# Kernel tuning notes

Hardware: AMD Instinct MI355X
Metric: run time of the kernel (lower is better)

Reference implementation:

```python
import jax, jax.numpy as jnp
import numpy as np

N_STATE = 1024
N_HEAD = 16
DIM_PER_HEAD = N_STATE // N_HEAD  # 64
QK_SCALE = DIM_PER_HEAD ** (-0.5)
B, T, T_CACHE = 8, 256, 768


def setup_inputs() -> dict:
    key = jax.random.key(0)
    ks = jax.random.split(key, 12)
    s = 0.02
    return {
        "x": jax.random.normal(ks[0], (B, T, N_STATE), dtype=jnp.float32),
        "qk_mask": jnp.zeros((T, T_CACHE + T), dtype=jnp.float32),
        "cache_k": jax.random.normal(ks[1], (B, T_CACHE, N_STATE), dtype=jnp.float32),
        "cache_v": jax.random.normal(ks[2], (B, T_CACHE, N_STATE), dtype=jnp.float32),
        "Wq": jax.random.normal(ks[3], (N_STATE, N_STATE), dtype=jnp.float32) * s,
        "bq": jax.random.normal(ks[4], (N_STATE,), dtype=jnp.float32) * s,
        "Wk": jax.random.normal(ks[5], (N_STATE, N_STATE), dtype=jnp.float32) * s,
        "Wv": jax.random.normal(ks[6], (N_STATE, N_STATE), dtype=jnp.float32) * s,
        "bv": jax.random.normal(ks[7], (N_STATE,), dtype=jnp.float32) * s,
        "Wo": jax.random.normal(ks[8], (N_STATE, N_STATE), dtype=jnp.float32) * s,
        "bo": jax.random.normal(ks[9], (N_STATE,), dtype=jnp.float32) * s,
    }


def reference(x, qk_mask, cache_k, cache_v, Wq, bq, Wk, Wv, bv, Wo, bo):
    # Linear projections (weights stored as [in, out], i.e. torch weight^T)
    q = (x @ Wq + bq) * QK_SCALE            # [B, T, D]
    new_k = x @ Wk                           # key has no bias
    new_v = x @ Wv + bv
    # KV-cache concat along time
    k = jnp.concatenate([cache_k, new_k], axis=1)  # [B, Tkv, D]
    v = jnp.concatenate([cache_v, new_v], axis=1)
    # Split heads
    Bq, Tq = q.shape[:2]
    Tkv = k.shape[1]
    qh = q.reshape(Bq, Tq, N_HEAD, DIM_PER_HEAD)    # [B, T, H, d]
    kh = k.reshape(Bq, Tkv, N_HEAD, DIM_PER_HEAD)
    vh = v.reshape(Bq, Tkv, N_HEAD, DIM_PER_HEAD)
    # q @ k^T + mask, softmax over keys
    qk = jnp.einsum("bthd,bshd->bhts", qh, kh) + qk_mask  # [B, H, T, Tkv]
    w = jax.nn.softmax(qk, axis=-1).astype(qh.dtype)
    wv = jnp.einsum("bhts,bshd->bthd", w, vh).reshape(Bq, Tq, N_STATE)
    out = wv @ Wo + bo
    return out, new_k, new_v
```

## Files before the change

kernel.cpp:

```cpp
#include <hip/hip_runtime.h>
#include <hip/hip_bf16.h>
#include <stdint.h>

#define Bb 8
#define Tt 256
#define TCC 768
#define TKV 1024
#define NS 1024
#define NH 16
#define DH 64
#define QK_SCALE 0.125f

typedef short bf16x8 __attribute__((ext_vector_type(8)));
typedef float f32x4 __attribute__((ext_vector_type(4)));

__device__ __forceinline__ unsigned short f2bf(float f) {
  union { float f; uint32_t u; } v; v.f = f;
  uint32_t u = v.u;
  u += 0x7fff + ((u >> 16) & 1);
  return (unsigned short)(u >> 16);
}

__global__ void convert_flat(const float* __restrict__ x, const float* __restrict__ ck,
                             unsigned short* __restrict__ xb, unsigned short* __restrict__ kb) {
  const int64_t nx4 = (int64_t)Bb * Tt * NS / 4;
  const int64_t nk4 = (int64_t)Bb * TCC * NS / 4;
  int64_t stride = (int64_t)gridDim.x * blockDim.x;
  for (int64_t t = (int64_t)blockIdx.x * blockDim.x + threadIdx.x; t < nx4 + nk4; t += stride) {
    if (t < nx4) {
      float4 v = ((const float4*)x)[t];
      ushort4 o; o.x = f2bf(v.x); o.y = f2bf(v.y); o.z = f2bf(v.z); o.w = f2bf(v.w);
      ((ushort4*)xb)[t] = o;
    } else {
      int64_t e = t - nx4;
      float4 v = ((const float4*)ck)[e];
      ushort4 o; o.x = f2bf(v.x); o.y = f2bf(v.y); o.z = f2bf(v.z); o.w = f2bf(v.w);
      int64_t el = e * 4;
      int64_t b = el / ((int64_t)TCC * NS);
      int64_t rem = el % ((int64_t)TCC * NS);
      int64_t d = b * (int64_t)TKV * NS + rem;
      ((ushort4*)kb)[d / 4] = o;
    }
  }
}

__global__ void transpose_convert(const float* __restrict__ Wq, const float* __restrict__ Wk,
                                  const float* __restrict__ Wv, const float* __restrict__ Wo,
                                  const float* __restrict__ cv,
                                  unsigned short* __restrict__ wqt, unsigned short* __restrict__ wkt,
                                  unsigned short* __restrict__ wvt, unsigned short* __restrict__ wot,
                                  unsigned short* __restrict__ vbt) {
  __shared__ float tile[64][65];
  int bid = blockIdx.x;
  const float* src; unsigned short* dst;
  if (bid < 1024) {
    int mat = bid >> 8, t = bid & 255;
    int tr = t >> 4, tc = t & 15;
    const float* W = (mat == 0) ? Wq : (mat == 1) ? Wk : (mat == 2) ? Wv : Wo;
    unsigned short* Wt = (mat == 0) ? wqt : (mat == 1) ? wkt : (mat == 2) ? wvt : wot;
    src = W + (int64_t)(tr * 64) * 1024 + tc * 64;
    dst = Wt + (int64_t)(tc * 64) * 1024 + tr * 64;
  } else {
    int e = bid - 1024;
    int b = e / 192; int t = e % 192;
    int st = t >> 4, ct = t & 15;
    src = cv + (int64_t)b * TCC * NS + (int64_t)(st * 64) * 1024 + ct * 64;
    dst = vbt + (int64_t)b * NS * TKV + (int64_t)(ct * 64) * 1024 + st * 64;
  }
  for (int e = threadIdx.x; e < 4096; e += 256) {
    int i = e >> 6, j = e & 63;
    tile[i][j] = src[(int64_t)i * 1024 + j];
  }
  __syncthreads();
  for (int e = threadIdx.x; e < 4096; e += 256) {
    int i = e >> 6, j = e & 63;
    dst[(int64_t)i * 1024 + j] = f2bf(tile[j][i]);
  }
}

template <int MODE>
__global__ void gemm128(const unsigned short* __restrict__ A,
                        const unsigned short* __restrict__ Bt0, const unsigned short* __restrict__ Bt1,
                        const unsigned short* __restrict__ Bt2,
                        const float* __restrict__ bq, const float* __restrict__ bv,
                        const float* __restrict__ bo,
                        unsigned short* __restrict__ qb,
                        float* __restrict__ okf, float* __restrict__ ovf,
                        unsigned short* __restrict__ kb, unsigned short* __restrict__ vbt,
                        float* __restrict__ outf) {
  __shared__ unsigned short As[128 * 40];
  __shared__ unsigned short Bs[128 * 40];
  int tid = threadIdx.x, lane = tid & 63, w = tid >> 6;
  int lr = lane & 15, hi = lane >> 4;
  int wr = w >> 1, wc = w & 1;

  int tm, seg, col0;
  const unsigned short* Bt;
  if (MODE == 0) {
    tm = blockIdx.x & 15; int tn = blockIdx.x >> 4;
    seg = tn >> 3; col0 = (tn & 7) * 128;
    Bt = (seg == 0) ? Bt0 : (seg == 1) ? Bt1 : Bt2;
  } else {
    tm = blockIdx.x & 15; int tn = blockIdx.x >> 4;
    seg = 0; col0 = tn * 128;
    Bt = Bt0;
  }
  int m0 = tm * 128;

  f32x4 acc[4][4];
#pragma unroll
  for (int i = 0; i < 4; i++)
#pragma unroll
    for (int j = 0; j < 4; j++) acc[i][j] = (f32x4){0.f, 0.f, 0.f, 0.f};

  for (int k0 = 0; k0 < 1024; k0 += 32) {
#pragma unroll
    for (int e = tid; e < 512; e += 256) {
      int r = e >> 2, kc = (e & 3) * 8;
      *(bf16x8*)&As[r * 40 + kc] = *(const bf16x8*)&A[(int64_t)(m0 + r) * 1024 + k0 + kc];
      *(bf16x8*)&Bs[r * 40 + kc] = *(const bf16x8*)&Bt[(int64_t)(col0 + r) * 1024 + k0 + kc];
    }
    __syncthreads();
    bf16x8 af[4], bf[4];
#pragma unroll
    for (int mt = 0; mt < 4; mt++) af[mt] = *(const bf16x8*)&As[(wr * 64 + mt * 16 + lr) * 40 + hi * 8];
#pragma unroll
    for (int nt = 0; nt < 4; nt++) bf[nt] = *(const bf16x8*)&Bs[(wc * 64 + nt * 16 + lr) * 40 + hi * 8];
#pragma unroll
    for (int mt = 0; mt < 4; mt++)
#pragma unroll
      for (int nt = 0; nt < 4; nt++)
        acc[mt][nt] = __builtin_amdgcn_mfma_f32_16x16x32_bf16(af[mt], bf[nt], acc[mt][nt], 0, 0, 0);
    __syncthreads();
  }

#pragma unroll
  for (int mt = 0; mt < 4; mt++)
#pragma unroll
    for (int nt = 0; nt < 4; nt++) {
      int row = m0 + wr * 64 + mt * 16 + hi * 4;
      int col = col0 + wc * 64 + nt * 16 + lr;
      if (MODE == 1) {
        float bias = bo[col];
#pragma unroll
        for (int r = 0; r < 4; r++)
          outf[(int64_t)(row + r) * 1024 + col] = acc[mt][nt][r] + bias;
      } else if (seg == 0) {
        float bias = bq[col];
#pragma unroll
        for (int r = 0; r < 4; r++)
          qb[(int64_t)(row + r) * 1024 + col] = f2bf((acc[mt][nt][r] + bias) * QK_SCALE);
      } else if (seg == 1) {
#pragma unroll
        for (int r = 0; r < 4; r++) {
          float v = acc[mt][nt][r];
          okf[(int64_t)(row + r) * 1024 + col] = v;
          int b = (row + r) >> 8, t = (row + r) & 255;
          kb[((int64_t)(b * TKV + TCC + t)) * 1024 + col] = f2bf(v);
        }
      } else {
        float bias = bv[col];
        int b = row >> 8, t0 = row & 255;
        int64_t voff = ((int64_t)(b * NH + (col >> 6)) * DH + (col & 63)) * TKV + TCC + t0;
        ushort4 pk;
        float v0 = acc[mt][nt][0] + bias, v1 = acc[mt][nt][1] + bias,
              v2 = acc[mt][nt][2] + bias, v3 = acc[mt][nt][3] + bias;
        ovf[(int64_t)(row + 0) * 1024 + col] = v0;
        ovf[(int64_t)(row + 1) * 1024 + col] = v1;
        ovf[(int64_t)(row + 2) * 1024 + col] = v2;
        ovf[(int64_t)(row + 3) * 1024 + col] = v3;
        pk.x = f2bf(v0); pk.y = f2bf(v1); pk.z = f2bf(v2); pk.w = f2bf(v3);
        *(ushort4*)&vbt[voff] = pk;
      }
    }
}

__global__ void attn(const unsigned short* __restrict__ qb, const unsigned short* __restrict__ kb,
                     const unsigned short* __restrict__ vbt, const float* __restrict__ mask,
                     unsigned short* __restrict__ wvb) {
  __shared__ unsigned short Ks[64 * 72];
  __shared__ unsigned short Vs[64 * 72];
  __shared__ unsigned short Ps[4][16 * 72];
  int tid = threadIdx.x, lane = tid & 63, w = tid >> 6;
  int lr = lane & 15, hi = lane >> 4;
  int qblk = blockIdx.x & 3, bh = blockIdx.x >> 2, b = bh >> 4, h = bh & 15;
  int q0 = qblk * 64 + w * 16;

  const unsigned short* qp = qb + ((int64_t)(b * Tt + q0 + lr)) * 1024 + h * DH + hi * 8;
  bf16x8 aq0 = *(const bf16x8*)qp;
  bf16x8 aq1 = *(const bf16x8*)(qp + 32);

  f32x4 o[4];
#pragma unroll
  for (int nt = 0; nt < 4; nt++) o[nt] = (f32x4){0.f, 0.f, 0.f, 0.f};
  float m[4] = {-1e30f, -1e30f, -1e30f, -1e30f};
  float l[4] = {0.f, 0.f, 0.f, 0.f};

  const unsigned short* kbase = kb + (int64_t)b * TKV * 1024 + h * DH;
  const unsigned short* vbase = vbt + (int64_t)bh * DH * TKV;
  const float* mbase = mask + (int64_t)(q0 + hi * 4) * TKV;

  for (int c = 0; c < 16; c++) {
    int kv0 = c * 64;
#pragma unroll
    for (int e = tid; e < 512; e += 256) {
      int r = e >> 3, kc = (e & 7) * 8;
      *(bf16x8*)&Ks[r * 72 + kc] = *(const bf16x8*)&kbase[(int64_t)(kv0 + r) * 1024 + kc];
      *(bf16x8*)&Vs[r * 72 + kc] = *(const bf16x8*)&vbase[(int64_t)r * TKV + kv0 + kc];
    }
    __syncthreads();

    f32x4 s[4];
#pragma unroll
    for (int nt = 0; nt < 4; nt++) {
      bf16x8 bk0 = *(const bf16x8*)&Ks[(nt * 16 + lr) * 72 + hi * 8];
      bf16x8 bk1 = *(const bf16x8*)&Ks[(nt * 16 + lr) * 72 + 32 + hi * 8];
      f32x4 z = (f32x4){0.f, 0.f, 0.f, 0.f};
      z = __builtin_amdgcn_mfma_f32_16x16x32_bf16(aq0, bk0, z, 0, 0, 0);
      z = __builtin_amdgcn_mfma_f32_16x16x32_bf16(aq1, bk1, z, 0, 0, 0);
      s[nt] = z;
    }
#pragma unroll
    for (int nt = 0; nt < 4; nt++)
#pragma unroll
      for (int r = 0; r < 4; r++)
        s[nt][r] += mbase[(int64_t)r * TKV + kv0 + nt * 16 + lr];

    float cm[4];
#pragma unroll
    for (int r = 0; r < 4; r++) {
      cm[r] = fmaxf(fmaxf(s[0][r], s[1][r]), fmaxf(s[2][r], s[3][r]));
#pragma unroll
      for (int d = 1; d < 16; d <<= 1) cm[r] = fmaxf(cm[r], __shfl_xor(cm[r], d));
    }
    float al[4], rs[4];
#pragma unroll
    for (int r = 0; r < 4; r++) {
      float nm = fmaxf(m[r], cm[r]);
      al[r] = __expf(m[r] - nm);
      m[r] = nm;
      rs[r] = 0.f;
    }
#pragma unroll
    for (int nt = 0; nt < 4; nt++)
#pragma unroll
      for (int r = 0; r < 4; r++) {
        s[nt][r] = __expf(s[nt][r] - m[r]);
        rs[r] += s[nt][r];
      }
#pragma unroll
    for (int r = 0; r < 4; r++) {
#pragma unroll
      for (int d = 1; d < 16; d <<= 1) rs[r] += __shfl_xor(rs[r], d);
      l[r] = l[r] * al[r] + rs[r];
    }
#pragma unroll
    for (int nt = 0; nt < 4; nt++)
#pragma unroll
      for (int r = 0; r < 4; r++) o[nt][r] *= al[r];

#pragma unroll
    for (int nt = 0; nt < 4; nt++)
#pragma unroll
      for (int r = 0; r < 4; r++)
        Ps[w][(hi * 4 + r) * 72 + nt * 16 + lr] = f2bf(s[nt][r]);
    __syncthreads();

    bf16x8 pa0 = *(const bf16x8*)&Ps[w][lr * 72 + hi * 8];
    bf16x8 pa1 = *(const bf16x8*)&Ps[w][lr * 72 + 32 + hi * 8];
#pragma unroll
    for (int nt = 0; nt < 4; nt++) {
      bf16x8 bv0 = *(const bf16x8*)&Vs[(nt * 16 + lr) * 72 + hi * 8];
      bf16x8 bv1 = *(const bf16x8*)&Vs[(nt * 16 + lr) * 72 + 32 + hi * 8];
      o[nt] = __builtin_amdgcn_mfma_f32_16x16x32_bf16(pa0, bv0, o[nt], 0, 0, 0);
      o[nt] = __builtin_amdgcn_mfma_f32_16x16x32_bf16(pa1, bv1, o[nt], 0, 0, 0);
    }
    __syncthreads();
  }

  float inv[4];
#pragma unroll
  for (int r = 0; r < 4; r++) inv[r] = 1.f / l[r];
#pragma unroll
  for (int nt = 0; nt < 4; nt++)
#pragma unroll
    for (int r = 0; r < 4; r++)
      wvb[(int64_t)(b * Tt + q0 + hi * 4 + r) * 1024 + h * DH + nt * 16 + lr] =
          f2bf(o[nt][r] * inv[r]);
}

extern "C" void kernel_launch(void* const* d_in, const int* in_sizes, int n_in,
                              void* d_out, int out_size, void* d_ws, size_t ws_size,
                              hipStream_t stream) {
  const float* x    = (const float*)d_in[0];
  const float* mask = (const float*)d_in[1];
  const float* ck   = (const float*)d_in[2];
  const float* cv   = (const float*)d_in[3];
  const float* Wq   = (const float*)d_in[4];
  const float* bq   = (const float*)d_in[5];
  const float* Wk   = (const float*)d_in[6];
  const float* Wv   = (const float*)d_in[7];
  const float* bv   = (const float*)d_in[8];
  const float* Wo   = (const float*)d_in[9];
  const float* bo   = (const float*)d_in[10];

  const int64_t NT = (int64_t)Bb * Tt * NS;
  float* outp = (float*)d_out;
  float* okf  = outp + NT;
  float* ovf  = outp + 2 * NT;

  char* ws = (char*)d_ws;
  unsigned short* xb  = (unsigned short*)(ws);
  unsigned short* wqt = (unsigned short*)(ws + (4LL << 20));
  unsigned short* wkt = (unsigned short*)(ws + (6LL << 20));
  unsigned short* wvt = (unsigned short*)(ws + (8LL << 20));
  unsigned short* wot = (unsigned short*)(ws + (10LL << 20));
  unsigned short* qbw = (unsigned short*)(ws + (12LL << 20));
  unsigned short* kbw = (unsigned short*)(ws + (16LL << 20));
  unsigned short* vbt = (unsigned short*)(ws + (32LL << 20));
  unsigned short* wvb = (unsigned short*)(ws + (48LL << 20));

  convert_flat<<<2048, 256, 0, stream>>>(x, ck, xb, kbw);
  transpose_convert<<<2560, 256, 0, stream>>>(Wq, Wk, Wv, Wo, cv, wqt, wkt, wvt, wot, vbt);
  gemm128<0><<<384, 256, 0, stream>>>(xb, wqt, wkt, wvt, bq, bv, bo,
                                      qbw, okf, ovf, kbw, vbt, outp);
  attn<<<512, 256, 0, stream>>>(qbw, kbw, vbt, mask, wvb);
  gemm128<1><<<128, 256, 0, stream>>>(wvb, wot, wot, wot, bq, bv, bo,
                                      qbw, okf, ovf, kbw, vbt, outp);
}
```

Before: 242.7 us.

## Split attention over KV across waves, use direct-to-LDS GEMM loads, vectorize transposes

Attention now gives each block 16 queries and has each of its four waves take a quarter of the KV range, loading K and V fragments straight from global memory. The partial max, sum and output of each wave are merged through shared memory at the end, which removes the per-chunk LDS staging and barriers. The GEMMs use global_load_lds to write tiles directly into unpadded LDS, and the output projection uses 64-row tiles to launch more blocks. The transpose kernel moves to float4 reads and ushort4 writes, and s_setprio is added around the MFMA sections. Unpadded LDS can cause bank conflicts, and per-wave global loads give up reuse of K and V across the waves of a block.

Result: slower. 248.9 us (+2.6%).

```diff
diff --git a/kernel.cpp b/kernel.cpp
--- a/kernel.cpp
+++ b/kernel.cpp
@@ -13,6 +13,7 @@
 
 typedef short bf16x8 __attribute__((ext_vector_type(8)));
 typedef float f32x4 __attribute__((ext_vector_type(4)));
+typedef unsigned int u32;
 
 __device__ __forceinline__ unsigned short f2bf(float f) {
   union { float f; uint32_t u; } v; v.f = f;
@@ -21,8 +22,16 @@
   return (unsigned short)(u >> 16);
 }
 
-__global__ void convert_flat(const float* __restrict__ x, const float* __restrict__ ck,
-                             unsigned short* __restrict__ xb, unsigned short* __restrict__ kb) {
+__device__ __forceinline__ void gload16(const unsigned short* g, unsigned short* l) {
+  __builtin_amdgcn_global_load_lds(
+      (__attribute__((address_space(1))) u32*)g,
+      (__attribute__((address_space(3))) u32*)l,
+      16, 0, 0);
+}
+
+__global__ __launch_bounds__(256) void convert_flat(
+    const float* __restrict__ x, const float* __restrict__ ck,
+    unsigned short* __restrict__ xb, unsigned short* __restrict__ kb) {
   const int64_t nx4 = (int64_t)Bb * Tt * NS / 4;
   const int64_t nk4 = (int64_t)Bb * TCC * NS / 4;
   int64_t stride = (int64_t)gridDim.x * blockDim.x;
@@ -44,12 +53,13 @@
   }
 }
 
-__global__ void transpose_convert(const float* __restrict__ Wq, const float* __restrict__ Wk,
-                                  const float* __restrict__ Wv, const float* __restrict__ Wo,
-                                  const float* __restrict__ cv,
-                                  unsigned short* __restrict__ wqt, unsigned short* __restrict__ wkt,
-                                  unsigned short* __restrict__ wvt, unsigned short* __restrict__ wot,
-                                  unsigned short* __restrict__ vbt) {
+__global__ __launch_bounds__(256) void transpose_convert(
+    const float* __restrict__ Wq, const float* __restrict__ Wk,
+    const float* __restrict__ Wv, const float* __restrict__ Wo,
+    const float* __restrict__ cv,
+    unsigned short* __restrict__ wqt, unsigned short* __restrict__ wkt,
+    unsigned short* __restrict__ wvt, unsigned short* __restrict__ wot,
+    unsigned short* __restrict__ vbt) {
   __shared__ float tile[64][65];
   int bid = blockIdx.x;
   const float* src; unsigned short* dst;
@@ -67,79 +77,95 @@
     src = cv + (int64_t)b * TCC * NS + (int64_t)(st * 64) * 1024 + ct * 64;
     dst = vbt + (int64_t)b * NS * TKV + (int64_t)(ct * 64) * 1024 + st * 64;
   }
-  for (int e = threadIdx.x; e < 4096; e += 256) {
-    int i = e >> 6, j = e & 63;
-    tile[i][j] = src[(int64_t)i * 1024 + j];
+  for (int e = threadIdx.x; e < 1024; e += 256) {
+    int i = e >> 4, j4 = (e & 15) * 4;
+    float4 v = *(const float4*)&src[(int64_t)i * 1024 + j4];
+    tile[i][j4] = v.x; tile[i][j4 + 1] = v.y; tile[i][j4 + 2] = v.z; tile[i][j4 + 3] = v.w;
   }
   __syncthreads();
-  for (int e = threadIdx.x; e < 4096; e += 256) {
-    int i = e >> 6, j = e & 63;
-    dst[(int64_t)i * 1024 + j] = f2bf(tile[j][i]);
+  for (int e = threadIdx.x; e < 1024; e += 256) {
+    int i = e >> 4, j4 = (e & 15) * 4;
+    ushort4 o;
+    o.x = f2bf(tile[j4][i]); o.y = f2bf(tile[j4 + 1][i]);
+    o.z = f2bf(tile[j4 + 2][i]); o.w = f2bf(tile[j4 + 3][i]);
+    *(ushort4*)&dst[(int64_t)i * 1024 + j4] = o;
   }
 }
 
 template <int MODE>
-__global__ void gemm128(const unsigned short* __restrict__ A,
-                        const unsigned short* __restrict__ Bt0, const unsigned short* __restrict__ Bt1,
-                        const unsigned short* __restrict__ Bt2,
-                        const float* __restrict__ bq, const float* __restrict__ bv,
-                        const float* __restrict__ bo,
-                        unsigned short* __restrict__ qb,
-                        float* __restrict__ okf, float* __restrict__ ovf,
-                        unsigned short* __restrict__ kb, unsigned short* __restrict__ vbt,
-                        float* __restrict__ outf) {
-  __shared__ unsigned short As[128 * 40];
-  __shared__ unsigned short Bs[128 * 40];
+__global__ __launch_bounds__(256) void gemm_mfma(
+    const unsigned short* __restrict__ A,
+    const unsigned short* __restrict__ Bt0, const unsigned short* __restrict__ Bt1,
+    const unsigned short* __restrict__ Bt2,
+    const float* __restrict__ bq, const float* __restrict__ bv,
+    const float* __restrict__ bo,
+    unsigned short* __restrict__ qb,
+    float* __restrict__ okf, float* __restrict__ ovf,
+    unsigned short* __restrict__ kb, unsigned short* __restrict__ vbt,
+    float* __restrict__ outf) {
+  constexpr int BM = (MODE == 0) ? 128 : 64;
+  constexpr int NT = (MODE == 0) ? 4 : 2;
+  __shared__ __align__(16) unsigned short As[BM * 32];
+  __shared__ __align__(16) unsigned short Bs[128 * 32];
   int tid = threadIdx.x, lane = tid & 63, w = tid >> 6;
   int lr = lane & 15, hi = lane >> 4;
-  int wr = w >> 1, wc = w & 1;
-
-  int tm, seg, col0;
+  int wr = (MODE == 0) ? (w >> 1) : 0;
+  int colw = (MODE == 0) ? ((w & 1) * 64) : (w * 32);
+
+  int tm, tn, seg, col0;
   const unsigned short* Bt;
   if (MODE == 0) {
-    tm = blockIdx.x & 15; int tn = blockIdx.x >> 4;
+    tm = blockIdx.x & 15; tn = blockIdx.x >> 4;
     seg = tn >> 3; col0 = (tn & 7) * 128;
     Bt = (seg == 0) ? Bt0 : (seg == 1) ? Bt1 : Bt2;
   } else {
-    tm = blockIdx.x & 15; int tn = blockIdx.x >> 4;
+    tm = blockIdx.x & 31; tn = blockIdx.x >> 5;
     seg = 0; col0 = tn * 128;
     Bt = Bt0;
   }
-  int m0 = tm * 128;
-
-  f32x4 acc[4][4];
+  int m0 = tm * BM;
+
+  f32x4 acc[4][NT];
 #pragma unroll
   for (int i = 0; i < 4; i++)
 #pragma unroll
-    for (int j = 0; j < 4; j++) acc[i][j] = (f32x4){0.f, 0.f, 0.f, 0.f};
+    for (int j = 0; j < NT; j++) acc[i][j] = (f32x4){0.f, 0.f, 0.f, 0.f};
 
   for (int k0 = 0; k0 < 1024; k0 += 32) {
 #pragma unroll
-    for (int e = tid; e < 512; e += 256) {
-      int r = e >> 2, kc = (e & 3) * 8;
-      *(bf16x8*)&As[r * 40 + kc] = *(const bf16x8*)&A[(int64_t)(m0 + r) * 1024 + k0 + kc];
-      *(bf16x8*)&Bs[r * 40 + kc] = *(const bf16x8*)&Bt[(int64_t)(col0 + r) * 1024 + k0 + kc];
+    for (int i = 0; i < BM / 64; i++) {
+      int slot = i * 256 + tid;
+      int r = slot >> 2, c = (slot & 3) * 8;
+      gload16(&A[(int64_t)(m0 + r) * 1024 + k0 + c], &As[slot * 8]);
+    }
+#pragma unroll
+    for (int i = 0; i < 2; i++) {
+      int slot = i * 256 + tid;
+      int r = slot >> 2, c = (slot & 3) * 8;
+      gload16(&Bt[(int64_t)(col0 + r) * 1024 + k0 + c], &Bs[slot * 8]);
     }
     __syncthreads();
-    bf16x8 af[4], bf[4];
-#pragma unroll
-    for (int mt = 0; mt < 4; mt++) af[mt] = *(const bf16x8*)&As[(wr * 64 + mt * 16 + lr) * 40 + hi * 8];
-#pragma unroll
-    for (int nt = 0; nt < 4; nt++) bf[nt] = *(const bf16x8*)&Bs[(wc * 64 + nt * 16 + lr) * 40 + hi * 8];
+    bf16x8 af[4], bfr[NT];
 #pragma unroll
     for (int mt = 0; mt < 4; mt++)
-#pragma unroll
-      for (int nt = 0; nt < 4; nt++)
-        acc[mt][nt] = __builtin_amdgcn_mfma_f32_16x16x32_bf16(af[mt], bf[nt], acc[mt][nt], 0, 0, 0);
+      af[mt] = *(const bf16x8*)&As[(wr * 64 + mt * 16 + lr) * 32 + hi * 8];
+#pragma unroll
+    for (int nt = 0; nt < NT; nt++)
+      bfr[nt] = *(const bf16x8*)&Bs[(colw + nt * 16 + lr) * 32 + hi * 8];
+#pragma unroll
+    for (int mt = 0; mt < 4; mt++)
+#pragma unroll
+      for (int nt = 0; nt < NT; nt++)
+        acc[mt][nt] = __builtin_amdgcn_mfma_f32_16x16x32_bf16(af[mt], bfr[nt], acc[mt][nt], 0, 0, 0);
     __syncthreads();
   }
 
 #pragma unroll
   for (int mt = 0; mt < 4; mt++)
 #pragma unroll
-    for (int nt = 0; nt < 4; nt++) {
+    for (int nt = 0; nt < NT; nt++) {
       int row = m0 + wr * 64 + mt * 16 + hi * 4;
-      int col = col0 + wc * 64 + nt * 16 + lr;
+      int col = col0 + colw + nt * 16 + lr;
       if (MODE == 1) {
         float bias = bo[col];
 #pragma unroll
@@ -162,29 +188,33 @@
         float bias = bv[col];
         int b = row >> 8, t0 = row & 255;
         int64_t voff = ((int64_t)(b * NH + (col >> 6)) * DH + (col & 63)) * TKV + TCC + t0;
-        ushort4 pk;
         float v0 = acc[mt][nt][0] + bias, v1 = acc[mt][nt][1] + bias,
               v2 = acc[mt][nt][2] + bias, v3 = acc[mt][nt][3] + bias;
         ovf[(int64_t)(row + 0) * 1024 + col] = v0;
         ovf[(int64_t)(row + 1) * 1024 + col] = v1;
         ovf[(int64_t)(row + 2) * 1024 + col] = v2;
         ovf[(int64_t)(row + 3) * 1024 + col] = v3;
-        pk.x = f2bf(v0); pk.y = f2bf(v1); pk.z = f2bf(v2); pk.w = f2bf(v3);
+        ushort4 pk; pk.x = f2bf(v0); pk.y = f2bf(v1); pk.z = f2bf(v2); pk.w = f2bf(v3);
         *(ushort4*)&vbt[voff] = pk;
       }
     }
 }
 
-__global__ void attn(const unsigned short* __restrict__ qb, const unsigned short* __restrict__ kb,
-                     const unsigned short* __restrict__ vbt, const float* __restrict__ mask,
-                     unsigned short* __restrict__ wvb) {
-  __shared__ unsigned short Ks[64 * 72];
-  __shared__ unsigned short Vs[64 * 72];
-  __shared__ unsigned short Ps[4][16 * 72];
+__global__ __launch_bounds__(256) void attn(
+    const unsigned short* __restrict__ qb, const unsigned short* __restrict__ kb,
+    const unsigned short* __restrict__ vbt, const float* __restrict__ mask,
+    unsigned short* __restrict__ wvb) {
+  __shared__ __align__(16) float OshF[4 * 16 * 64];
+  __shared__ float Msh[4][16];
+  __shared__ float Lsh[4][16];
+  unsigned short* Ps = (unsigned short*)OshF;
+
   int tid = threadIdx.x, lane = tid & 63, w = tid >> 6;
   int lr = lane & 15, hi = lane >> 4;
-  int qblk = blockIdx.x & 3, bh = blockIdx.x >> 2, b = bh >> 4, h = bh & 15;
-  int q0 = qblk * 64 + w * 16;
+  int bid = blockIdx.x;
+  int logical = (bid & 7) * 256 + (bid >> 3);
+  int qt = logical & 15, bh = logical >> 4, b = bh >> 4, h = bh & 15;
+  int q0 = qt * 16;
 
   const unsigned short* qp = qb + ((int64_t)(b * Tt + q0 + lr)) * 1024 + h * DH + hi * 8;
   bf16x8 aq0 = *(const bf16x8*)qp;
@@ -200,26 +230,30 @@
   const unsigned short* vbase = vbt + (int64_t)bh * DH * TKV;
   const float* mbase = mask + (int64_t)(q0 + hi * 4) * TKV;
 
-  for (int c = 0; c < 16; c++) {
-    int kv0 = c * 64;
-#pragma unroll
-    for (int e = tid; e < 512; e += 256) {
-      int r = e >> 3, kc = (e & 7) * 8;
-      *(bf16x8*)&Ks[r * 72 + kc] = *(const bf16x8*)&kbase[(int64_t)(kv0 + r) * 1024 + kc];
-      *(bf16x8*)&Vs[r * 72 + kc] = *(const bf16x8*)&vbase[(int64_t)r * TKV + kv0 + kc];
-    }
-    __syncthreads();
+  for (int ci = 0; ci < 4; ci++) {
+    int kv0 = (w * 4 + ci) * 64;
+    bf16x8 bk0[4], bk1[4], bv0[4], bv1[4];
+#pragma unroll
+    for (int nt = 0; nt < 4; nt++) {
+      const unsigned short* kr = &kbase[(int64_t)(kv0 + nt * 16 + lr) * 1024 + hi * 8];
+      bk0[nt] = *(const bf16x8*)kr;
+      bk1[nt] = *(const bf16x8*)(kr + 32);
+      const unsigned short* vr = &vbase[(int64_t)(nt * 16 + lr) * TKV + kv0 + hi * 8];
+      bv0[nt] = *(const bf16x8*)vr;
+      bv1[nt] = *(const bf16x8*)(vr + 32);
+    }
 
     f32x4 s[4];
+    __builtin_amdgcn_s_setprio(1);
 #pragma unroll
     for (int nt = 0; nt < 4; nt++) {
-      bf16x8 bk0 = *(const bf16x8*)&Ks[(nt * 16 + lr) * 72 + hi * 8];
-      bf16x8 bk1 = *(const bf16x8*)&Ks[(nt * 16 + lr) * 72 + 32 + hi * 8];
       f32x4 z = (f32x4){0.f, 0.f, 0.f, 0.f};
-      z = __builtin_amdgcn_mfma_f32_16x16x32_bf16(aq0, bk0, z, 0, 0, 0);
-      z = __builtin_amdgcn_mfma_f32_16x16x32_bf16(aq1, bk1, z, 0, 0, 0);
+      z = __builtin_amdgcn_mfma_f32_16x16x32_bf16(aq0, bk0[nt], z, 0, 0, 0);
+      z = __builtin_amdgcn_mfma_f32_16x16x32_bf16(aq1, bk1[nt], z, 0, 0, 0);
       s[nt] = z;
     }
+    __builtin_amdgcn_s_setprio(0);
+
 #pragma unroll
     for (int nt = 0; nt < 4; nt++)
 #pragma unroll
@@ -263,30 +297,53 @@
     for (int nt = 0; nt < 4; nt++)
 #pragma unroll
       for (int r = 0; r < 4; r++)
-        Ps[w][(hi * 4 + r) * 72 + nt * 16 + lr] = f2bf(s[nt][r]);
-    __syncthreads();
-
-    bf16x8 pa0 = *(const bf16x8*)&Ps[w][lr * 72 + hi * 8];
-    bf16x8 pa1 = *(const bf16x8*)&Ps[w][lr * 72 + 32 + hi * 8];
+        Ps[w * 1216 + (hi * 4 + r) * 76 + nt * 16 + lr] = f2bf(s[nt][r]);
+    bf16x8 pa0 = *(const bf16x8*)&Ps[w * 1216 + lr * 76 + hi * 8];
+    bf16x8 pa1 = *(const bf16x8*)&Ps[w * 1216 + lr * 76 + 32 + hi * 8];
+
+    __builtin_amdgcn_s_setprio(1);
 #pragma unroll
     for (int nt = 0; nt < 4; nt++) {
-      bf16x8 bv0 = *(const bf16x8*)&Vs[(nt * 16 + lr) * 72 + hi * 8];
-      bf16x8 bv1 = *(const bf16x8*)&Vs[(nt * 16 + lr) * 72 + 32 + hi * 8];
-      o[nt] = __builtin_amdgcn_mfma_f32_16x16x32_bf16(pa0, bv0, o[nt], 0, 0, 0);
-      o[nt] = __builtin_amdgcn_mfma_f32_16x16x32_bf16(pa1, bv1, o[nt], 0, 0, 0);
-    }
-    __syncthreads();
-  }
-
-  float inv[4];
-#pragma unroll
-  for (int r = 0; r < 4; r++) inv[r] = 1.f / l[r];
+      o[nt] = __builtin_amdgcn_mfma_f32_16x16x32_bf16(pa0, bv0[nt], o[nt], 0, 0, 0);
+      o[nt] = __builtin_amdgcn_mfma_f32_16x16x32_bf16(pa1, bv1[nt], o[nt], 0, 0, 0);
+    }
+    __builtin_amdgcn_s_setprio(0);
+  }
+
+  if (lr == 0) {
+#pragma unroll
+    for (int r = 0; r < 4; r++) { Msh[w][hi * 4 + r] = m[r]; Lsh[w][hi * 4 + r] = l[r]; }
+  }
+  __syncthreads();
+  float fw[4];
+#pragma unroll
+  for (int r = 0; r < 4; r++) {
+    int row = hi * 4 + r;
+    float M = fmaxf(fmaxf(Msh[0][row], Msh[1][row]), fmaxf(Msh[2][row], Msh[3][row]));
+    fw[r] = __expf(m[r] - M);
+  }
+  float* Osh = OshF + w * 1024;
 #pragma unroll
   for (int nt = 0; nt < 4; nt++)
 #pragma unroll
     for (int r = 0; r < 4; r++)
-      wvb[(int64_t)(b * Tt + q0 + hi * 4 + r) * 1024 + h * DH + nt * 16 + lr] =
-          f2bf(o[nt][r] * inv[r]);
+      Osh[(hi * 4 + r) * 64 + nt * 16 + lr] = o[nt][r] * fw[r];
+  __syncthreads();
+  {
+    int row = tid >> 4, d0 = (tid & 15) * 4;
+    float M = fmaxf(fmaxf(Msh[0][row], Msh[1][row]), fmaxf(Msh[2][row], Msh[3][row]));
+    float lsum = Lsh[0][row] * __expf(Msh[0][row] - M) + Lsh[1][row] * __expf(Msh[1][row] - M) +
+                 Lsh[2][row] * __expf(Msh[2][row] - M) + Lsh[3][row] * __expf(Msh[3][row] - M);
+    float inv = 1.f / lsum;
+    float v[4];
+#pragma unroll
+    for (int t = 0; t < 4; t++) {
+      int idx = row * 64 + d0 + t;
+      v[t] = (OshF[idx] + OshF[1024 + idx] + OshF[2048 + idx] + OshF[3072 + idx]) * inv;
+    }
+    ushort4 pk; pk.x = f2bf(v[0]); pk.y = f2bf(v[1]); pk.z = f2bf(v[2]); pk.w = f2bf(v[3]);
+    *(ushort4*)&wvb[(int64_t)(b * Tt + q0 + row) * 1024 + h * DH + d0] = pk;
+  }
 }
 
 extern "C" void kernel_launch(void* const* d_in, const int* in_sizes, int n_in,
@@ -322,9 +379,9 @@
 
   convert_flat<<<2048, 256, 0, stream>>>(x, ck, xb, kbw);
   transpose_convert<<<2560, 256, 0, stream>>>(Wq, Wk, Wv, Wo, cv, wqt, wkt, wvt, wot, vbt);
-  gemm128<0><<<384, 256, 0, stream>>>(xb, wqt, wkt, wvt, bq, bv, bo,
-                                      qbw, okf, ovf, kbw, vbt, outp);
-  attn<<<512, 256, 0, stream>>>(qbw, kbw, vbt, mask, wvb);
-  gemm128<1><<<128, 256, 0, stream>>>(wvb, wot, wot, wot, bq, bv, bo,
-                                      qbw, okf, ovf, kbw, vbt, outp);
-}
+  gemm_mfma<0><<<384, 256, 0, stream>>>(xb, wqt, wkt, wvt, bq, bv, bo,
+                                        qbw, okf, ovf, kbw, vbt, outp);
+  attn<<<2048, 256, 0, stream>>>(qbw, kbw, vbt, mask, wvb);
+  gemm_mfma<1><<<256, 256, 0, stream>>>(wvb, wot, wot, wot, bq, bv, bo,
+                                        qbw, okf, ovf, kbw, vbt, outp);
+}
```
